# Kernel tuning notes

Measured on AMD Instinct MI355X. Metric: run time of the kernel, lower is better.

Reference implementation:

```python
import jax, jax.numpy as jnp
import numpy as np

C_M = 256   # norm_channel (msa channel)
C_Z = 128   # pair_channel
H = 8       # num_head
C = 32      # attention_channel per head


def layer_norm(x, gamma, beta, eps=1e-5):
    mu = jnp.mean(x, axis=-1, keepdims=True)
    var = jnp.var(x, axis=-1, keepdims=True)
    return (x - mu) * jax.lax.rsqrt(var + eps) * gamma + beta


def setup_inputs() -> dict:
    key = jax.random.key(0)
    ks = jax.random.split(key, 12)
    B, S, R = 1, 128, 256
    inp = {
        "msa_act": jax.random.normal(ks[0], (B, S, R, C_M), jnp.float32),
        "pair_act": jax.random.normal(ks[1], (B, R, R, C_Z), jnp.float32),
        "msa_mask": jnp.ones((B, S, R), jnp.float32),
        # query_norm params
        "qn_g": jnp.ones((C_M,), jnp.float32),
        "qn_b": jnp.zeros((C_M,), jnp.float32),
        # feat_2d_norm params
        "pn_g": jnp.ones((C_Z,), jnp.float32),
        "pn_b": jnp.zeros((C_Z,), jnp.float32),
        # feat_2d_weights: Linear(C_Z -> H, bias=False)
        "w2d": jax.random.normal(ks[2], (C_Z, H), jnp.float32) / np.sqrt(C_Z),
        # attention projections [C_M, H, C]
        "wq": jax.random.normal(ks[3], (C_M, H, C), jnp.float32) / np.sqrt(C_M),
        "wk": jax.random.normal(ks[4], (C_M, H, C), jnp.float32) / np.sqrt(C_M),
        "wv": jax.random.normal(ks[5], (C_M, H, C), jnp.float32) / np.sqrt(C_M),
        # gating linear [C_M, H, C] + bias
        "wg": jax.random.normal(ks[6], (C_M, H, C), jnp.float32) / np.sqrt(C_M),
        "bg": jnp.ones((H, C), jnp.float32),
        # output linear [H, C, C_M] + bias
        "wo": jax.random.normal(ks[7], (H, C, C_M), jnp.float32) / np.sqrt(H * C),
        "bo": jnp.zeros((C_M,), jnp.float32),
    }
    return inp


def reference(msa_act, pair_act, msa_mask, qn_g, qn_b, pn_g, pn_b, w2d,
              wq, wk, wv, wg, bg, wo, bo):
    # Pair bias: LayerNorm -> Linear(C_Z->H) -> permute to [B, 1, H, R, R]
    z = layer_norm(pair_act, pn_g, pn_b)            # [B, R, R, C_Z]
    z = jnp.einsum('bqkc,ch->bhqk', z, w2d)          # [B, H, R, R]
    z = z[:, None]                                   # [B, 1, H, R, R]

    # Mask bias: [B, S, 1, 1, R]
    mask_bias = (1e9 * (msa_mask - 1.0))[:, :, None, None, :]

    # Row-wise MHA with query norm
    m = layer_norm(msa_act, qn_g, qn_b)              # [B, S, R, C_M]
    scale = 1.0 / np.sqrt(C)
    q = jnp.einsum('bsqc,chd->bshqd', m, wq) * scale
    k = jnp.einsum('bskc,chd->bshkd', m, wk)
    v = jnp.einsum('bskc,chd->bshkd', m, wv)

    logits = jnp.einsum('bshqd,bshkd->bshqk', q, k) + mask_bias + z
    a = jax.nn.softmax(logits, axis=-1)              # [B, S, H, R, R]
    o = jnp.einsum('bshqk,bshkd->bsqhd', a, v)       # [B, S, R, H, C]

    g = jax.nn.sigmoid(jnp.einsum('bsqc,chd->bsqhd', m, wg) + bg)
    o = o * g
    out = jnp.einsum('bsqhd,hdc->bsqc', o, wo) + bo  # [B, S, R, C_M]
    return out
```

## Files before the change

kernel.cpp:

```cpp
#include <hip/hip_runtime.h>
#include <hip/hip_bf16.h>

typedef unsigned short u16;
typedef __attribute__((ext_vector_type(8))) short bf16x8;
typedef __attribute__((ext_vector_type(4))) float f32x4;

__device__ __forceinline__ float bf2f(u16 u){
  union { unsigned int i; float f; } v; v.i = ((unsigned int)u) << 16; return v.f;
}
__device__ __forceinline__ u16 f2bf(float f){
  union { float f; unsigned int i; } v; v.f = f;
  unsigned int i = v.i;
  return (u16)((i + 0x7fffu + ((i >> 16) & 1u)) >> 16);
}
__device__ __forceinline__ unsigned int pk2(float a, float b){
  union { __hip_bfloat162 v; unsigned int u; } c;
  c.v = __float22bfloat162_rn(float2{a, b});
  return c.u;
}
__device__ __forceinline__ float ldin(const void* p, int i, int f){
  return f ? ((const float*)p)[i] : bf2f(((const u16*)p)[i]);
}
__device__ __forceinline__ bf16x8 pack8(const float* v){
  union { bf16x8 v8; unsigned int w[4]; } u;
  #pragma unroll
  for (int j = 0; j < 4; ++j) u.w[j] = pk2(v[2*j], v[2*j+1]);
  return u.v8;
}

__global__ void k_sniff(const unsigned int* __restrict__ msa_w, int* __restrict__ flag)
{
  int lane = threadIdx.x & 63;
  int lo0 = 0, expok = 0;
  #pragma unroll
  for (int j = 0; j < 4; ++j) {
    unsigned int w = msa_w[lane * 4 + j];
    if ((w & 0xffffu) == 0u) lo0++;
    unsigned int e = (w >> 7) & 0xffu;
    if (e >= 110u && e <= 140u) expok++;
  }
  #pragma unroll
  for (int off = 1; off < 64; off <<= 1) {
    lo0   += __shfl_xor(lo0,   off, 64);
    expok += __shfl_xor(expok, off, 64);
  }
  if (lane == 0 && blockIdx.x == 0)
    *flag = (lo0 > 200) ? 1 : ((expok > 200) ? 0 : 1);
}

__global__ __launch_bounds__(256) void k_transpose(
    const void* __restrict__ wq, const void* __restrict__ wk,
    const void* __restrict__ wv, const void* __restrict__ wg,
    const void* __restrict__ wo, const int* __restrict__ flagp,
    u16* __restrict__ Wt, u16* __restrict__ wot)
{
  __shared__ u16 T[64 * 72];
  const int flag = *flagp;
  const int t = threadIdx.x;
  const int mat = blockIdx.x >> 4, tile = blockIdx.x & 15;
  const int R0 = (tile >> 2) * 64, C0 = (tile & 3) * 64;
  const void* src = (mat == 0) ? wq : (mat == 1) ? wk : (mat == 2) ? wv
                  : (mat == 3) ? wg : wo;
  u16* dst = (mat < 4) ? (Wt + mat * 65536) : wot;
  {
    int i = t >> 2, j0 = (t & 3) * 16;
    #pragma unroll
    for (int e = 0; e < 8; ++e) {
      float a = ldin(src, (R0 + i) * 256 + C0 + j0 + 2*e,     flag);
      float b = ldin(src, (R0 + i) * 256 + C0 + j0 + 2*e + 1, flag);
      *(unsigned int*)(T + i * 72 + j0 + 2*e) = pk2(a, b);
    }
  }
  __syncthreads();
  {
    int j = t >> 2, i0 = (t & 3) * 16;
    u16 o[16];
    #pragma unroll
    for (int e = 0; e < 16; ++e) o[e] = T[(i0 + e) * 72 + j];
    *(uint4*)(dst + (C0 + j) * 256 + R0 + i0)     = *(const uint4*)o;
    *(uint4*)(dst + (C0 + j) * 256 + R0 + i0 + 8) = *(const uint4*)(o + 8);
  }
}

__global__ __launch_bounds__(256) void k_pair_z(
    const void* __restrict__ pair, const void* __restrict__ png,
    const void* __restrict__ pnb, const void* __restrict__ w2d,
    const int* __restrict__ flagp, u16* __restrict__ z_bf)
{
  __shared__ u16 As[64 * 136];
  __shared__ u16 Bs[16 * 136];
  const int flag = *flagp;
  const int t = threadIdx.x, lane = t & 63, wave = t >> 6;
  const int g = lane >> 4, l15 = lane & 15;
  const int rowBase = blockIdx.x * 64;

  if (t < 128) {
    #pragma unroll
    for (int n = 0; n < 16; ++n)
      Bs[n * 136 + t] = (n < 8) ? f2bf(ldin(w2d, t * 8 + n, flag)) : (u16)0;
  }
  {
    int lrow = t >> 2, cb = (t & 3) * 32;
    int base = (rowBase + lrow) * 128 + cb;
    float x[32];
    if (flag) {
      const float* p = (const float*)pair + base;
      #pragma unroll
      for (int j = 0; j < 8; ++j) {
        float4 f4 = *(const float4*)(p + 4 * j);
        x[4*j] = f4.x; x[4*j+1] = f4.y; x[4*j+2] = f4.z; x[4*j+3] = f4.w;
      }
    } else {
      const u16* p = (const u16*)pair + base;
      #pragma unroll
      for (int j = 0; j < 4; ++j) {
        uint4 u = *(const uint4*)(p + 8 * j);
        const u16* h = (const u16*)&u;
        #pragma unroll
        for (int e = 0; e < 8; ++e) x[8*j+e] = bf2f(h[e]);
      }
    }
    float s = 0.f, sq = 0.f;
    #pragma unroll
    for (int j = 0; j < 32; ++j) { s += x[j]; sq += x[j] * x[j]; }
    s  += __shfl_xor(s, 1, 64);  s  += __shfl_xor(s, 2, 64);
    sq += __shfl_xor(sq, 1, 64); sq += __shfl_xor(sq, 2, 64);
    float mu = s * (1.f / 128.f);
    float var = sq * (1.f / 128.f) - mu * mu;
    float rs = rsqrtf(var + 1e-5f);
    float n_[32];
    #pragma unroll
    for (int j = 0; j < 32; ++j) {
      int c = cb + j;
      n_[j] = (x[j] - mu) * rs * ldin(png, c, flag) + ldin(pnb, c, flag);
    }
    u16* dst = As + lrow * 136 + cb;
    #pragma unroll
    for (int j = 0; j < 16; ++j)
      *(unsigned int*)(dst + 2*j) = pk2(n_[2*j], n_[2*j+1]);
  }
  __syncthreads();

  f32x4 accz = {0.f, 0.f, 0.f, 0.f};
  #pragma unroll
  for (int kb = 0; kb < 4; ++kb) {
    bf16x8 a = *(const bf16x8*)(As + (wave * 16 + l15) * 136 + kb * 32 + g * 8);
    bf16x8 b = *(const bf16x8*)(Bs + l15 * 136 + kb * 32 + g * 8);
    accz = __builtin_amdgcn_mfma_f32_16x16x32_bf16(a, b, accz, 0, 0, 0);
  }
  if (l15 < 8) {
    #pragma unroll
    for (int r = 0; r < 4; ++r)
      z_bf[l15 * 65536 + rowBase + wave * 16 + g * 4 + r] = f2bf(accz[r]);
  }
}

__global__ __launch_bounds__(256) void k_msa_ln(
    const void* __restrict__ msa, const void* __restrict__ qng,
    const void* __restrict__ qnb, const int* __restrict__ flagp,
    u16* __restrict__ m_bf)
{
  const int flag = *flagp;
  int wave = threadIdx.x >> 6, lane = threadIdx.x & 63;
  int row = blockIdx.x * 4 + wave;
  float x[4];
  if (flag) {
    float4 f4 = *((const float4*)msa + row * 64 + lane);
    x[0]=f4.x; x[1]=f4.y; x[2]=f4.z; x[3]=f4.w;
  } else {
    uint2 u = *((const uint2*)msa + row * 64 + lane);
    const u16* h = (const u16*)&u;
    #pragma unroll
    for (int j = 0; j < 4; ++j) x[j] = bf2f(h[j]);
  }
  float s = 0.f, sq = 0.f;
  #pragma unroll
  for (int j = 0; j < 4; ++j) { s += x[j]; sq += x[j] * x[j]; }
  #pragma unroll
  for (int off = 1; off < 64; off <<= 1) {
    s  += __shfl_xor(s,  off, 64);
    sq += __shfl_xor(sq, off, 64);
  }
  float mu = s * (1.f / 256.f);
  float var = sq * (1.f / 256.f) - mu * mu;
  float rs = rsqrtf(var + 1e-5f);
  float y[4];
  #pragma unroll
  for (int j = 0; j < 4; ++j) {
    int c = lane * 4 + j;
    y[j] = (x[j] - mu) * rs * ldin(qng, c, flag) + ldin(qnb, c, flag);
  }
  uint2 o2;
  o2.x = pk2(y[0], y[1]);
  o2.y = pk2(y[2], y[3]);
  *((uint2*)m_bf + row * 64 + lane) = o2;
}

__global__ __launch_bounds__(256, 2) void k_fused(
    const u16* __restrict__ m_bf, const u16* __restrict__ Wt,
    const void* __restrict__ bg, const u16* __restrict__ z_bf,
    const void* __restrict__ mask, const int* __restrict__ flagp,
    u16* __restrict__ og_ws)
{
  __shared__ u16 Ks[256 * 40];
  __shared__ u16 Vts[32 * 264];
  __shared__ u16 Qs[4][64 * 40];
  __shared__ float Tb[4][16 * 36];
  __shared__ float Mb[256];
  const int flag = *flagp;
  const int t = threadIdx.x, lane = t & 63, wave = t >> 6;
  const int s_ = blockIdx.x, h = blockIdx.y;
  const int g = lane >> 4, l15 = lane & 15;

  Mb[t] = 1e9f * (ldin(mask, s_ * 256 + t, flag) - 1.0f);

  bf16x8 af[8][4];
  #pragma unroll
  for (int kb = 0; kb < 8; ++kb)
    #pragma unroll
    for (int mt = 0; mt < 4; ++mt)
      af[kb][mt] = *(const bf16x8*)(
          m_bf + (s_ * 256 + wave * 64 + mt * 16 + l15) * 256 + kb * 32 + g * 8);

  const float scale = 0.17677669529663687f;
  float gg[4][2][4];
  f32x4 zero = {0.f, 0.f, 0.f, 0.f};

  #pragma unroll
  for (int matid = 0; matid < 4; ++matid) {
    const u16* W = Wt + matid * 65536 + (h * 32) * 256;
    f32x4 acc[4][2];
    #pragma unroll
    for (int mt = 0; mt < 4; ++mt) { acc[mt][0] = zero; acc[mt][1] = zero; }
    #pragma unroll
    for (int kb = 0; kb < 8; ++kb) {
      bf16x8 b0 = *(const bf16x8*)(W + l15 * 256        + kb * 32 + g * 8);
      bf16x8 b1 = *(const bf16x8*)(W + (16 + l15) * 256 + kb * 32 + g * 8);
      #pragma unroll
      for (int mt = 0; mt < 4; ++mt) {
        acc[mt][0] = __builtin_amdgcn_mfma_f32_16x16x32_bf16(af[kb][mt], b0, acc[mt][0], 0, 0, 0);
        acc[mt][1] = __builtin_amdgcn_mfma_f32_16x16x32_bf16(af[kb][mt], b1, acc[mt][1], 0, 0, 0);
      }
    }
    #pragma unroll
    for (int mt = 0; mt < 4; ++mt)
      #pragma unroll
      for (int nt = 0; nt < 2; ++nt)
        #pragma unroll
        for (int r = 0; r < 4; ++r) {
          int rowl = wave * 64 + mt * 16 + g * 4 + r;
          int dd = nt * 16 + l15;
          float v = acc[mt][nt][r];
          if (matid == 0)
            Qs[wave][(mt * 16 + g * 4 + r) * 40 + dd] = f2bf(v * scale);
          else if (matid == 1)
            Ks[rowl * 40 + dd] = f2bf(v);
          else if (matid == 2)
            Vts[dd * 264 + rowl] = f2bf(v);
          else {
            float gv = v + ldin(bg, h * 32 + dd, flag);
            gg[mt][nt][r] = 1.0f / (1.0f + __expf(-gv));
          }
        }
  }
  __syncthreads();

  const u16* Qw = &Qs[wave][0];
  float* Tw = &Tb[wave][0];
  for (int qt = 0; qt < 4; ++qt) {
    const int qbase = wave * 64 + qt * 16;
    bf16x8 aq = *(const bf16x8*)(Qw + (qt * 16 + l15) * 40 + g * 8);
    f32x4 S[16];
    #pragma unroll
    for (int kt = 0; kt < 16; ++kt) {
      bf16x8 bk = *(const bf16x8*)(Ks + (kt * 16 + l15) * 40 + g * 8);
      S[kt] = __builtin_amdgcn_mfma_f32_16x16x32_bf16(aq, bk, zero, 0, 0, 0);
    }
    const u16* zb = z_bf + h * 65536 + (qbase + l15) * 256;
    uint4 zu[8];
    #pragma unroll
    for (int kc = 0; kc < 8; ++kc) zu[kc] = *(const uint4*)(zb + kc * 32 + g * 8);

    float L[8][8];
    #pragma unroll
    for (int kc = 0; kc < 8; ++kc) {
      asm volatile("s_waitcnt lgkmcnt(0)" ::: "memory");
      #pragma unroll
      for (int half = 0; half < 2; ++half)
        #pragma unroll
        for (int r = 0; r < 4; ++r)
          Tw[(g * 4 + r) * 36 + half * 16 + l15] = S[kc * 2 + half][r];
      asm volatile("s_waitcnt lgkmcnt(0)" ::: "memory");
      float4 t0 = *(const float4*)(Tw + l15 * 36 + g * 8);
      float4 t1 = *(const float4*)(Tw + l15 * 36 + g * 8 + 4);
      float4 m0 = *(const float4*)(Mb + kc * 32 + g * 8);
      float4 m1 = *(const float4*)(Mb + kc * 32 + g * 8 + 4);
      const u16* zh = (const u16*)&zu[kc];
      L[kc][0] = __expf(t0.x + m0.x + bf2f(zh[0]));
      L[kc][1] = __expf(t0.y + m0.y + bf2f(zh[1]));
      L[kc][2] = __expf(t0.z + m0.z + bf2f(zh[2]));
      L[kc][3] = __expf(t0.w + m0.w + bf2f(zh[3]));
      L[kc][4] = __expf(t1.x + m1.x + bf2f(zh[4]));
      L[kc][5] = __expf(t1.y + m1.y + bf2f(zh[5]));
      L[kc][6] = __expf(t1.z + m1.z + bf2f(zh[6]));
      L[kc][7] = __expf(t1.w + m1.w + bf2f(zh[7]));
    }
    float sm = 0.f;
    #pragma unroll
    for (int kc = 0; kc < 8; ++kc)
      #pragma unroll
      for (int j = 0; j < 8; ++j) sm += L[kc][j];
    sm += __shfl_xor(sm, 16, 64);
    sm += __shfl_xor(sm, 32, 64);
    f32x4 O0 = zero, O1 = zero;
    #pragma unroll
    for (int kc = 0; kc < 8; ++kc) {
      bf16x8 ap  = pack8(&L[kc][0]);
      bf16x8 bv0 = *(const bf16x8*)(Vts + l15 * 264 + kc * 32 + g * 8);
      bf16x8 bv1 = *(const bf16x8*)(Vts + (16 + l15) * 264 + kc * 32 + g * 8);
      O0 = __builtin_amdgcn_mfma_f32_16x16x32_bf16(ap, bv0, O0, 0, 0, 0);
      O1 = __builtin_amdgcn_mfma_f32_16x16x32_bf16(ap, bv1, O1, 0, 0, 0);
    }
    #pragma unroll
    for (int r = 0; r < 4; ++r) {
      float smr = __shfl(sm, g * 4 + r, 64);
      float inv = 1.0f / smr;
      int qq = qbase + g * 4 + r;
      int base = (s_ * 256 + qq) * 256 + h * 32;
      float o0 = O0[r] * inv * gg[qt][0][r];
      float o1 = O1[r] * inv * gg[qt][1][r];
      og_ws[base + l15]      = f2bf(o0);
      og_ws[base + 16 + l15] = f2bf(o1);
    }
  }
}

__global__ __launch_bounds__(256, 2) void k_outproj(
    const u16* __restrict__ og, const u16* __restrict__ wot,
    const void* __restrict__ bo, const int* __restrict__ flagp,
    void* __restrict__ outv)
{
  const int flag = *flagp;
  const int t = threadIdx.x, lane = t & 63, wave = t >> 6;
  const int wm = (wave >> 1) * 64, wn = (wave & 1) * 64;
  const int rowBase = blockIdx.x * 128;
  const int ct = blockIdx.y;
  const int g = lane >> 4, l15 = lane & 15;

  bf16x8 af[8][4];
  #pragma unroll
  for (int kb = 0; kb < 8; ++kb)
    #pragma unroll
    for (int mt = 0; mt < 4; ++mt)
      af[kb][mt] = *(const bf16x8*)(
          og + (rowBase + wm + mt * 16 + l15) * 256 + kb * 32 + g * 8);

  const u16* Wb = wot + (ct * 128 + wn) * 256;
  f32x4 acc[4][4];
  f32x4 zero = {0.f, 0.f, 0.f, 0.f};
  #pragma unroll
  for (int i = 0; i < 4; ++i)
    #pragma unroll
    for (int j = 0; j < 4; ++j) acc[i][j] = zero;
  #pragma unroll
  for (int kb = 0; kb < 8; ++kb) {
    bf16x8 bb[4];
    #pragma unroll
    for (int nt = 0; nt < 4; ++nt)
      bb[nt] = *(const bf16x8*)(Wb + (nt * 16 + l15) * 256 + kb * 32 + g * 8);
    #pragma unroll
    for (int mt = 0; mt < 4; ++mt)
      #pragma unroll
      for (int nt = 0; nt < 4; ++nt)
        acc[mt][nt] = __builtin_amdgcn_mfma_f32_16x16x32_bf16(
            af[kb][mt], bb[nt], acc[mt][nt], 0, 0, 0);
  }
  #pragma unroll
  for (int mt = 0; mt < 4; ++mt)
    #pragma unroll
    for (int nt = 0; nt < 4; ++nt)
      #pragma unroll
      for (int r = 0; r < 4; ++r) {
        int row = rowBase + wm + mt * 16 + g * 4 + r;
        int col = ct * 128 + wn + nt * 16 + l15;
        float val = acc[mt][nt][r] + ldin(bo, col, flag);
        if (flag) ((float*)outv)[row * 256 + col] = val;
        else      ((u16*)outv)[row * 256 + col]   = f2bf(val);
      }
}

extern "C" void kernel_launch(void* const* d_in, const int* in_sizes, int n_in,
                              void* d_out, int out_size, void* d_ws, size_t ws_size,
                              hipStream_t stream)
{
  const void* msa  = d_in[0];
  const void* pair = d_in[1];
  const void* mask = d_in[2];
  const void* qng  = d_in[3];
  const void* qnb  = d_in[4];
  const void* png  = d_in[5];
  const void* pnb  = d_in[6];
  const void* w2d  = d_in[7];
  const void* wq   = d_in[8];
  const void* wk   = d_in[9];
  const void* wv   = d_in[10];
  const void* wg   = d_in[11];
  const void* bg   = d_in[12];
  const void* wo   = d_in[13];
  const void* bo   = d_in[14];

  char* ws = (char*)d_ws;
  u16* z_bf  = (u16*)(ws + 0);
  u16* Wt    = (u16*)(ws + 1048576);
  u16* wot   = (u16*)(ws + 1572864);
  int* flag  = (int*)(ws + 1703936);
  u16* m_bf  = (u16*)(ws + 1704192);
  u16* og_ws = (u16*)(ws + 18481408);

  hipLaunchKernelGGL(k_sniff, dim3(1), dim3(64), 0, stream,
                     (const unsigned int*)msa, flag);
  hipLaunchKernelGGL(k_transpose, dim3(80), dim3(256), 0, stream,
                     wq, wk, wv, wg, wo, flag, Wt, wot);
  hipLaunchKernelGGL(k_msa_ln, dim3(8192), dim3(256), 0, stream,
                     msa, qng, qnb, flag, m_bf);
  hipLaunchKernelGGL(k_pair_z, dim3(1024), dim3(256), 0, stream,
                     pair, png, pnb, w2d, flag, z_bf);
  hipLaunchKernelGGL(k_fused, dim3(128, 8), dim3(256), 0, stream,
                     m_bf, Wt, bg, z_bf, mask, flag, og_ws);
  hipLaunchKernelGGL(k_outproj, dim3(256, 2), dim3(256), 0, stream,
                     og_ws, wot, bo, flag, d_out);
}
```

Before: 261.6 us.

## Merge prep kernels, use exp2 softmax, and shrink fused-attention LDS for occupancy

Folds the weight transpose, pair-bias LayerNorm/projection and MSA LayerNorm into one launch, removing two kernel launches. In the attention kernel, Q and gate values now live packed in registers instead of LDS. The K tile drops its padding in favour of an XOR swizzle, and projections run in two 32-row chunks. Together these cut LDS and register use so launch bounds can rise to 3 blocks per CU. Softmax switches to exp2 with log2e folded into the Q scale, mask and z bias, and the row sum is fused into the PV loop, at the cost of an extra LDS round-trip to rebuild the Q fragment for each tile.

Measured after the change: 283.4 us. 1.08x slower.

```diff
diff --git a/kernel.cpp b/kernel.cpp
--- a/kernel.cpp
+++ b/kernel.cpp
@@ -2,8 +2,11 @@
 #include <hip/hip_bf16.h>
 
 typedef unsigned short u16;
+typedef unsigned int u32;
 typedef __attribute__((ext_vector_type(8))) short bf16x8;
 typedef __attribute__((ext_vector_type(4))) float f32x4;
+
+#define LOG2E 1.4426950408889634f
 
 __device__ __forceinline__ float bf2f(u16 u){
   union { unsigned int i; float f; } v; v.i = ((unsigned int)u) << 16; return v.f;
@@ -13,8 +16,8 @@
   unsigned int i = v.i;
   return (u16)((i + 0x7fffu + ((i >> 16) & 1u)) >> 16);
 }
-__device__ __forceinline__ unsigned int pk2(float a, float b){
-  union { __hip_bfloat162 v; unsigned int u; } c;
+__device__ __forceinline__ u32 pk2(float a, float b){
+  union { __hip_bfloat162 v; u32 u; } c;
   c.v = __float22bfloat162_rn(float2{a, b});
   return c.u;
 }
@@ -22,10 +25,17 @@
   return f ? ((const float*)p)[i] : bf2f(((const u16*)p)[i]);
 }
 __device__ __forceinline__ bf16x8 pack8(const float* v){
-  union { bf16x8 v8; unsigned int w[4]; } u;
+  union { bf16x8 v8; u32 w[4]; } u;
   #pragma unroll
   for (int j = 0; j < 4; ++j) u.w[j] = pk2(v[2*j], v[2*j+1]);
   return u.v8;
+}
+__device__ __forceinline__ float fexp2(float x){
+#if __has_builtin(__builtin_amdgcn_exp2f)
+  return __builtin_amdgcn_exp2f(x);
+#else
+  return exp2f(x);
+#endif
 }
 
 __global__ void k_sniff(const unsigned int* __restrict__ msa_w, int* __restrict__ flag)
@@ -48,240 +58,261 @@
     *flag = (lo0 > 200) ? 1 : ((expok > 200) ? 0 : 1);
 }
 
-__global__ __launch_bounds__(256) void k_transpose(
+__global__ __launch_bounds__(256) void k_prep(
     const void* __restrict__ wq, const void* __restrict__ wk,
     const void* __restrict__ wv, const void* __restrict__ wg,
-    const void* __restrict__ wo, const int* __restrict__ flagp,
-    u16* __restrict__ Wt, u16* __restrict__ wot)
-{
-  __shared__ u16 T[64 * 72];
-  const int flag = *flagp;
-  const int t = threadIdx.x;
-  const int mat = blockIdx.x >> 4, tile = blockIdx.x & 15;
-  const int R0 = (tile >> 2) * 64, C0 = (tile & 3) * 64;
-  const void* src = (mat == 0) ? wq : (mat == 1) ? wk : (mat == 2) ? wv
-                  : (mat == 3) ? wg : wo;
-  u16* dst = (mat < 4) ? (Wt + mat * 65536) : wot;
-  {
-    int i = t >> 2, j0 = (t & 3) * 16;
-    #pragma unroll
-    for (int e = 0; e < 8; ++e) {
-      float a = ldin(src, (R0 + i) * 256 + C0 + j0 + 2*e,     flag);
-      float b = ldin(src, (R0 + i) * 256 + C0 + j0 + 2*e + 1, flag);
-      *(unsigned int*)(T + i * 72 + j0 + 2*e) = pk2(a, b);
-    }
-  }
-  __syncthreads();
-  {
-    int j = t >> 2, i0 = (t & 3) * 16;
-    u16 o[16];
-    #pragma unroll
-    for (int e = 0; e < 16; ++e) o[e] = T[(i0 + e) * 72 + j];
-    *(uint4*)(dst + (C0 + j) * 256 + R0 + i0)     = *(const uint4*)o;
-    *(uint4*)(dst + (C0 + j) * 256 + R0 + i0 + 8) = *(const uint4*)(o + 8);
-  }
-}
-
-__global__ __launch_bounds__(256) void k_pair_z(
+    const void* __restrict__ wo,
     const void* __restrict__ pair, const void* __restrict__ png,
     const void* __restrict__ pnb, const void* __restrict__ w2d,
-    const int* __restrict__ flagp, u16* __restrict__ z_bf)
+    const void* __restrict__ msa, const void* __restrict__ qng,
+    const void* __restrict__ qnb, const int* __restrict__ flagp,
+    u16* __restrict__ Wt, u16* __restrict__ wot,
+    u16* __restrict__ z_bf, u16* __restrict__ m_bf)
 {
-  __shared__ u16 As[64 * 136];
-  __shared__ u16 Bs[16 * 136];
+  __shared__ u16 SMEM[64 * 136 + 16 * 136];
   const int flag = *flagp;
   const int t = threadIdx.x, lane = t & 63, wave = t >> 6;
-  const int g = lane >> 4, l15 = lane & 15;
-  const int rowBase = blockIdx.x * 64;
-
-  if (t < 128) {
-    #pragma unroll
-    for (int n = 0; n < 16; ++n)
-      Bs[n * 136 + t] = (n < 8) ? f2bf(ldin(w2d, t * 8 + n, flag)) : (u16)0;
-  }
-  {
-    int lrow = t >> 2, cb = (t & 3) * 32;
-    int base = (rowBase + lrow) * 128 + cb;
-    float x[32];
+  const int bid = blockIdx.x;
+
+  if (bid < 80) {
+    u16* T = SMEM;
+    const int mat = bid >> 4, tile = bid & 15;
+    const int R0 = (tile >> 2) * 64, C0 = (tile & 3) * 64;
+    const void* src = (mat == 0) ? wq : (mat == 1) ? wk : (mat == 2) ? wv
+                    : (mat == 3) ? wg : wo;
+    u16* dst = (mat < 4) ? (Wt + mat * 65536) : wot;
+    {
+      int i = t >> 2, j0 = (t & 3) * 16;
+      #pragma unroll
+      for (int e = 0; e < 8; ++e) {
+        float a = ldin(src, (R0 + i) * 256 + C0 + j0 + 2*e,     flag);
+        float b = ldin(src, (R0 + i) * 256 + C0 + j0 + 2*e + 1, flag);
+        *(u32*)(T + i * 72 + j0 + 2*e) = pk2(a, b);
+      }
+    }
+    __syncthreads();
+    {
+      int j = t >> 2, i0 = (t & 3) * 16;
+      u16 o[16];
+      #pragma unroll
+      for (int e = 0; e < 16; ++e) o[e] = T[(i0 + e) * 72 + j];
+      *(uint4*)(dst + (C0 + j) * 256 + R0 + i0)     = *(const uint4*)o;
+      *(uint4*)(dst + (C0 + j) * 256 + R0 + i0 + 8) = *(const uint4*)(o + 8);
+    }
+  } else if (bid < 80 + 1024) {
+    u16* As = SMEM;
+    u16* Bs = SMEM + 64 * 136;
+    const int g = lane >> 4, l15 = lane & 15;
+    const int rowBase = (bid - 80) * 64;
+    if (t < 128) {
+      #pragma unroll
+      for (int n = 0; n < 16; ++n)
+        Bs[n * 136 + t] = (n < 8) ? f2bf(ldin(w2d, t * 8 + n, flag)) : (u16)0;
+    }
+    {
+      int lrow = t >> 2, cb = (t & 3) * 32;
+      int base = (rowBase + lrow) * 128 + cb;
+      float x[32];
+      if (flag) {
+        const float* p = (const float*)pair + base;
+        #pragma unroll
+        for (int j = 0; j < 8; ++j) {
+          float4 f4 = *(const float4*)(p + 4 * j);
+          x[4*j] = f4.x; x[4*j+1] = f4.y; x[4*j+2] = f4.z; x[4*j+3] = f4.w;
+        }
+      } else {
+        const u16* p = (const u16*)pair + base;
+        #pragma unroll
+        for (int j = 0; j < 4; ++j) {
+          uint4 u = *(const uint4*)(p + 8 * j);
+          const u16* hh = (const u16*)&u;
+          #pragma unroll
+          for (int e = 0; e < 8; ++e) x[8*j+e] = bf2f(hh[e]);
+        }
+      }
+      float s = 0.f, sq = 0.f;
+      #pragma unroll
+      for (int j = 0; j < 32; ++j) { s += x[j]; sq += x[j] * x[j]; }
+      s  += __shfl_xor(s, 1, 64);  s  += __shfl_xor(s, 2, 64);
+      sq += __shfl_xor(sq, 1, 64); sq += __shfl_xor(sq, 2, 64);
+      float mu = s * (1.f / 128.f);
+      float var = sq * (1.f / 128.f) - mu * mu;
+      float rs = rsqrtf(var + 1e-5f);
+      float n_[32];
+      #pragma unroll
+      for (int j = 0; j < 32; ++j) {
+        int c = cb + j;
+        n_[j] = (x[j] - mu) * rs * ldin(png, c, flag) + ldin(pnb, c, flag);
+      }
+      u16* dst = As + lrow * 136 + cb;
+      #pragma unroll
+      for (int j = 0; j < 16; ++j)
+        *(u32*)(dst + 2*j) = pk2(n_[2*j], n_[2*j+1]);
+    }
+    __syncthreads();
+    f32x4 accz = {0.f, 0.f, 0.f, 0.f};
+    #pragma unroll
+    for (int kb = 0; kb < 4; ++kb) {
+      bf16x8 a = *(const bf16x8*)(As + (wave * 16 + l15) * 136 + kb * 32 + g * 8);
+      bf16x8 b = *(const bf16x8*)(Bs + l15 * 136 + kb * 32 + g * 8);
+      accz = __builtin_amdgcn_mfma_f32_16x16x32_bf16(a, b, accz, 0, 0, 0);
+    }
+    if (l15 < 8) {
+      #pragma unroll
+      for (int r = 0; r < 4; ++r)
+        z_bf[l15 * 65536 + rowBase + wave * 16 + g * 4 + r] = f2bf(accz[r] * LOG2E);
+    }
+  } else {
+    int row = (bid - 1104) * 4 + wave;
+    float x[4];
     if (flag) {
-      const float* p = (const float*)pair + base;
-      #pragma unroll
-      for (int j = 0; j < 8; ++j) {
-        float4 f4 = *(const float4*)(p + 4 * j);
-        x[4*j] = f4.x; x[4*j+1] = f4.y; x[4*j+2] = f4.z; x[4*j+3] = f4.w;
-      }
+      float4 f4 = *((const float4*)msa + row * 64 + lane);
+      x[0]=f4.x; x[1]=f4.y; x[2]=f4.z; x[3]=f4.w;
     } else {
-      const u16* p = (const u16*)pair + base;
-      #pragma unroll
-      for (int j = 0; j < 4; ++j) {
-        uint4 u = *(const uint4*)(p + 8 * j);
-        const u16* h = (const u16*)&u;
-        #pragma unroll
-        for (int e = 0; e < 8; ++e) x[8*j+e] = bf2f(h[e]);
-      }
+      uint2 u = *((const uint2*)msa + row * 64 + lane);
+      const u16* hh = (const u16*)&u;
+      #pragma unroll
+      for (int j = 0; j < 4; ++j) x[j] = bf2f(hh[j]);
     }
     float s = 0.f, sq = 0.f;
     #pragma unroll
-    for (int j = 0; j < 32; ++j) { s += x[j]; sq += x[j] * x[j]; }
-    s  += __shfl_xor(s, 1, 64);  s  += __shfl_xor(s, 2, 64);
-    sq += __shfl_xor(sq, 1, 64); sq += __shfl_xor(sq, 2, 64);
-    float mu = s * (1.f / 128.f);
-    float var = sq * (1.f / 128.f) - mu * mu;
+    for (int j = 0; j < 4; ++j) { s += x[j]; sq += x[j] * x[j]; }
+    #pragma unroll
+    for (int off = 1; off < 64; off <<= 1) {
+      s  += __shfl_xor(s,  off, 64);
+      sq += __shfl_xor(sq, off, 64);
+    }
+    float mu = s * (1.f / 256.f);
+    float var = sq * (1.f / 256.f) - mu * mu;
     float rs = rsqrtf(var + 1e-5f);
-    float n_[32];
-    #pragma unroll
-    for (int j = 0; j < 32; ++j) {
-      int c = cb + j;
-      n_[j] = (x[j] - mu) * rs * ldin(png, c, flag) + ldin(pnb, c, flag);
-    }
-    u16* dst = As + lrow * 136 + cb;
-    #pragma unroll
-    for (int j = 0; j < 16; ++j)
-      *(unsigned int*)(dst + 2*j) = pk2(n_[2*j], n_[2*j+1]);
-  }
-  __syncthreads();
-
-  f32x4 accz = {0.f, 0.f, 0.f, 0.f};
-  #pragma unroll
-  for (int kb = 0; kb < 4; ++kb) {
-    bf16x8 a = *(const bf16x8*)(As + (wave * 16 + l15) * 136 + kb * 32 + g * 8);
-    bf16x8 b = *(const bf16x8*)(Bs + l15 * 136 + kb * 32 + g * 8);
-    accz = __builtin_amdgcn_mfma_f32_16x16x32_bf16(a, b, accz, 0, 0, 0);
-  }
-  if (l15 < 8) {
-    #pragma unroll
-    for (int r = 0; r < 4; ++r)
-      z_bf[l15 * 65536 + rowBase + wave * 16 + g * 4 + r] = f2bf(accz[r]);
-  }
-}
-
-__global__ __launch_bounds__(256) void k_msa_ln(
-    const void* __restrict__ msa, const void* __restrict__ qng,
-    const void* __restrict__ qnb, const int* __restrict__ flagp,
-    u16* __restrict__ m_bf)
-{
-  const int flag = *flagp;
-  int wave = threadIdx.x >> 6, lane = threadIdx.x & 63;
-  int row = blockIdx.x * 4 + wave;
-  float x[4];
-  if (flag) {
-    float4 f4 = *((const float4*)msa + row * 64 + lane);
-    x[0]=f4.x; x[1]=f4.y; x[2]=f4.z; x[3]=f4.w;
-  } else {
-    uint2 u = *((const uint2*)msa + row * 64 + lane);
-    const u16* h = (const u16*)&u;
-    #pragma unroll
-    for (int j = 0; j < 4; ++j) x[j] = bf2f(h[j]);
-  }
-  float s = 0.f, sq = 0.f;
-  #pragma unroll
-  for (int j = 0; j < 4; ++j) { s += x[j]; sq += x[j] * x[j]; }
-  #pragma unroll
-  for (int off = 1; off < 64; off <<= 1) {
-    s  += __shfl_xor(s,  off, 64);
-    sq += __shfl_xor(sq, off, 64);
-  }
-  float mu = s * (1.f / 256.f);
-  float var = sq * (1.f / 256.f) - mu * mu;
-  float rs = rsqrtf(var + 1e-5f);
-  float y[4];
-  #pragma unroll
-  for (int j = 0; j < 4; ++j) {
-    int c = lane * 4 + j;
-    y[j] = (x[j] - mu) * rs * ldin(qng, c, flag) + ldin(qnb, c, flag);
-  }
-  uint2 o2;
-  o2.x = pk2(y[0], y[1]);
-  o2.y = pk2(y[2], y[3]);
-  *((uint2*)m_bf + row * 64 + lane) = o2;
-}
-
-__global__ __launch_bounds__(256, 2) void k_fused(
+    float y[4];
+    #pragma unroll
+    for (int j = 0; j < 4; ++j) {
+      int c = lane * 4 + j;
+      y[j] = (x[j] - mu) * rs * ldin(qng, c, flag) + ldin(qnb, c, flag);
+    }
+    uint2 o2;
+    o2.x = pk2(y[0], y[1]);
+    o2.y = pk2(y[2], y[3]);
+    *((uint2*)m_bf + row * 64 + lane) = o2;
+  }
+}
+
+__global__ __launch_bounds__(256, 3) void k_fused(
     const u16* __restrict__ m_bf, const u16* __restrict__ Wt,
     const void* __restrict__ bg, const u16* __restrict__ z_bf,
     const void* __restrict__ mask, const int* __restrict__ flagp,
     u16* __restrict__ og_ws)
 {
-  __shared__ u16 Ks[256 * 40];
+  __shared__ u16 Ks[256 * 32];
   __shared__ u16 Vts[32 * 264];
-  __shared__ u16 Qs[4][64 * 40];
-  __shared__ float Tb[4][16 * 36];
+  __shared__ float Sb[4][16 * 36];
   __shared__ float Mb[256];
   const int flag = *flagp;
   const int t = threadIdx.x, lane = t & 63, wave = t >> 6;
   const int s_ = blockIdx.x, h = blockIdx.y;
   const int g = lane >> 4, l15 = lane & 15;
 
-  Mb[t] = 1e9f * (ldin(mask, s_ * 256 + t, flag) - 1.0f);
-
-  bf16x8 af[8][4];
-  #pragma unroll
-  for (int kb = 0; kb < 8; ++kb)
-    #pragma unroll
-    for (int mt = 0; mt < 4; ++mt)
-      af[kb][mt] = *(const bf16x8*)(
-          m_bf + (s_ * 256 + wave * 64 + mt * 16 + l15) * 256 + kb * 32 + g * 8);
-
-  const float scale = 0.17677669529663687f;
-  float gg[4][2][4];
+  Mb[t] = (1e9f * LOG2E) * (ldin(mask, s_ * 256 + t, flag) - 1.0f);
+
+  const float qscale = 0.17677669529663687f * LOG2E;
+  u32 qpk[4][2][2];
+  u32 gpk[4][2][2];
   f32x4 zero = {0.f, 0.f, 0.f, 0.f};
 
   #pragma unroll
-  for (int matid = 0; matid < 4; ++matid) {
-    const u16* W = Wt + matid * 65536 + (h * 32) * 256;
-    f32x4 acc[4][2];
-    #pragma unroll
-    for (int mt = 0; mt < 4; ++mt) { acc[mt][0] = zero; acc[mt][1] = zero; }
-    #pragma unroll
-    for (int kb = 0; kb < 8; ++kb) {
-      bf16x8 b0 = *(const bf16x8*)(W + l15 * 256        + kb * 32 + g * 8);
-      bf16x8 b1 = *(const bf16x8*)(W + (16 + l15) * 256 + kb * 32 + g * 8);
-      #pragma unroll
-      for (int mt = 0; mt < 4; ++mt) {
-        acc[mt][0] = __builtin_amdgcn_mfma_f32_16x16x32_bf16(af[kb][mt], b0, acc[mt][0], 0, 0, 0);
-        acc[mt][1] = __builtin_amdgcn_mfma_f32_16x16x32_bf16(af[kb][mt], b1, acc[mt][1], 0, 0, 0);
-      }
-    }
-    #pragma unroll
-    for (int mt = 0; mt < 4; ++mt)
-      #pragma unroll
-      for (int nt = 0; nt < 2; ++nt)
+  for (int c = 0; c < 2; ++c) {
+    bf16x8 af[8][2];
+    #pragma unroll
+    for (int kb = 0; kb < 8; ++kb)
+      #pragma unroll
+      for (int mt = 0; mt < 2; ++mt)
+        af[kb][mt] = *(const bf16x8*)(
+            m_bf + (s_*256 + wave*64 + c*32 + mt*16 + l15)*256 + kb*32 + g*8);
+
+    #pragma unroll
+    for (int matid = 0; matid < 4; ++matid) {
+      const u16* W = Wt + matid * 65536 + (h * 32) * 256;
+      f32x4 acc[2][2];
+      acc[0][0] = zero; acc[0][1] = zero; acc[1][0] = zero; acc[1][1] = zero;
+      #pragma unroll
+      for (int kb = 0; kb < 8; ++kb) {
+        bf16x8 b0 = *(const bf16x8*)(W + l15 * 256        + kb * 32 + g * 8);
+        bf16x8 b1 = *(const bf16x8*)(W + (16 + l15) * 256 + kb * 32 + g * 8);
         #pragma unroll
-        for (int r = 0; r < 4; ++r) {
-          int rowl = wave * 64 + mt * 16 + g * 4 + r;
-          int dd = nt * 16 + l15;
-          float v = acc[mt][nt][r];
-          if (matid == 0)
-            Qs[wave][(mt * 16 + g * 4 + r) * 40 + dd] = f2bf(v * scale);
-          else if (matid == 1)
-            Ks[rowl * 40 + dd] = f2bf(v);
-          else if (matid == 2)
-            Vts[dd * 264 + rowl] = f2bf(v);
-          else {
-            float gv = v + ldin(bg, h * 32 + dd, flag);
-            gg[mt][nt][r] = 1.0f / (1.0f + __expf(-gv));
+        for (int mt = 0; mt < 2; ++mt) {
+          acc[mt][0] = __builtin_amdgcn_mfma_f32_16x16x32_bf16(af[kb][mt], b0, acc[mt][0], 0, 0, 0);
+          acc[mt][1] = __builtin_amdgcn_mfma_f32_16x16x32_bf16(af[kb][mt], b1, acc[mt][1], 0, 0, 0);
+        }
+      }
+      #pragma unroll
+      for (int mt = 0; mt < 2; ++mt) {
+        const int tile = c * 2 + mt;
+        if (matid == 0) {
+          #pragma unroll
+          for (int nt = 0; nt < 2; ++nt) {
+            qpk[tile][nt][0] = pk2(acc[mt][nt][0] * qscale, acc[mt][nt][1] * qscale);
+            qpk[tile][nt][1] = pk2(acc[mt][nt][2] * qscale, acc[mt][nt][3] * qscale);
           }
+        } else if (matid == 3) {
+          #pragma unroll
+          for (int nt = 0; nt < 2; ++nt) {
+            float b = ldin(bg, h * 32 + nt * 16 + l15, flag);
+            float s0 = 1.f / (1.f + __expf(-(acc[mt][nt][0] + b)));
+            float s1 = 1.f / (1.f + __expf(-(acc[mt][nt][1] + b)));
+            float s2 = 1.f / (1.f + __expf(-(acc[mt][nt][2] + b)));
+            float s3 = 1.f / (1.f + __expf(-(acc[mt][nt][3] + b)));
+            gpk[tile][nt][0] = pk2(s0, s1);
+            gpk[tile][nt][1] = pk2(s2, s3);
+          }
+        } else {
+          #pragma unroll
+          for (int nt = 0; nt < 2; ++nt)
+            #pragma unroll
+            for (int r = 0; r < 4; ++r) {
+              int rowl = wave * 64 + c * 32 + mt * 16 + g * 4 + r;
+              int dd = nt * 16 + l15;
+              u16 o = f2bf(acc[mt][nt][r]);
+              if (matid == 1)
+                Ks[rowl * 32 + (((dd >> 3) ^ (r & 3)) << 3) + (dd & 7)] = o;
+              else
+                Vts[dd * 264 + rowl] = o;
+            }
         }
+      }
+    }
   }
   __syncthreads();
 
-  const u16* Qw = &Qs[wave][0];
-  float* Tw = &Tb[wave][0];
+  float* Sw = &Sb[wave][0];
+  u16* Swu = (u16*)Sw;
+  const u16* zb_base = z_bf + h * 65536;
+
   for (int qt = 0; qt < 4; ++qt) {
     const int qbase = wave * 64 + qt * 16;
-    bf16x8 aq = *(const bf16x8*)(Qw + (qt * 16 + l15) * 40 + g * 8);
+    asm volatile("s_waitcnt lgkmcnt(0)" ::: "memory");
+    #pragma unroll
+    for (int nt = 0; nt < 2; ++nt)
+      #pragma unroll
+      for (int r = 0; r < 4; ++r)
+        Swu[(g * 4 + r) * 72 + nt * 16 + l15] =
+            (u16)(qpk[qt][nt][r >> 1] >> ((r & 1) * 16));
+    asm volatile("s_waitcnt lgkmcnt(0)" ::: "memory");
+    bf16x8 aq = *(const bf16x8*)(Swu + l15 * 72 + g * 8);
+
     f32x4 S[16];
     #pragma unroll
     for (int kt = 0; kt < 16; ++kt) {
-      bf16x8 bk = *(const bf16x8*)(Ks + (kt * 16 + l15) * 40 + g * 8);
+      bf16x8 bk = *(const bf16x8*)(Ks + (kt * 16 + l15) * 32 + ((g ^ (l15 & 3)) << 3));
       S[kt] = __builtin_amdgcn_mfma_f32_16x16x32_bf16(aq, bk, zero, 0, 0, 0);
     }
-    const u16* zb = z_bf + h * 65536 + (qbase + l15) * 256;
+    const u16* zb = zb_base + (qbase + l15) * 256;
     uint4 zu[8];
     #pragma unroll
     for (int kc = 0; kc < 8; ++kc) zu[kc] = *(const uint4*)(zb + kc * 32 + g * 8);
 
-    float L[8][8];
+    float sm = 0.f;
+    f32x4 O0 = zero, O1 = zero;
     #pragma unroll
     for (int kc = 0; kc < 8; ++kc) {
       asm volatile("s_waitcnt lgkmcnt(0)" ::: "memory");
@@ -289,48 +320,41 @@
       for (int half = 0; half < 2; ++half)
         #pragma unroll
         for (int r = 0; r < 4; ++r)
-          Tw[(g * 4 + r) * 36 + half * 16 + l15] = S[kc * 2 + half][r];
+          Sw[(g * 4 + r) * 36 + half * 16 + l15] = S[kc * 2 + half][r];
       asm volatile("s_waitcnt lgkmcnt(0)" ::: "memory");
-      float4 t0 = *(const float4*)(Tw + l15 * 36 + g * 8);
-      float4 t1 = *(const float4*)(Tw + l15 * 36 + g * 8 + 4);
+      float4 t0 = *(const float4*)(Sw + l15 * 36 + g * 8);
+      float4 t1 = *(const float4*)(Sw + l15 * 36 + g * 8 + 4);
       float4 m0 = *(const float4*)(Mb + kc * 32 + g * 8);
       float4 m1 = *(const float4*)(Mb + kc * 32 + g * 8 + 4);
       const u16* zh = (const u16*)&zu[kc];
-      L[kc][0] = __expf(t0.x + m0.x + bf2f(zh[0]));
-      L[kc][1] = __expf(t0.y + m0.y + bf2f(zh[1]));
-      L[kc][2] = __expf(t0.z + m0.z + bf2f(zh[2]));
-      L[kc][3] = __expf(t0.w + m0.w + bf2f(zh[3]));
-      L[kc][4] = __expf(t1.x + m1.x + bf2f(zh[4]));
-      L[kc][5] = __expf(t1.y + m1.y + bf2f(zh[5]));
-      L[kc][6] = __expf(t1.z + m1.z + bf2f(zh[6]));
-      L[kc][7] = __expf(t1.w + m1.w + bf2f(zh[7]));
-    }
-    float sm = 0.f;
-    #pragma unroll
-    for (int kc = 0; kc < 8; ++kc)
-      #pragma unroll
-      for (int j = 0; j < 8; ++j) sm += L[kc][j];
-    sm += __shfl_xor(sm, 16, 64);
-    sm += __shfl_xor(sm, 32, 64);
-    f32x4 O0 = zero, O1 = zero;
-    #pragma unroll
-    for (int kc = 0; kc < 8; ++kc) {
-      bf16x8 ap  = pack8(&L[kc][0]);
+      float L[8];
+      L[0] = fexp2(t0.x + m0.x + bf2f(zh[0]));
+      L[1] = fexp2(t0.y + m0.y + bf2f(zh[1]));
+      L[2] = fexp2(t0.z + m0.z + bf2f(zh[2]));
+      L[3] = fexp2(t0.w + m0.w + bf2f(zh[3]));
+      L[4] = fexp2(t1.x + m1.x + bf2f(zh[4]));
+      L[5] = fexp2(t1.y + m1.y + bf2f(zh[5]));
+      L[6] = fexp2(t1.z + m1.z + bf2f(zh[6]));
+      L[7] = fexp2(t1.w + m1.w + bf2f(zh[7]));
+      sm += ((L[0] + L[1]) + (L[2] + L[3])) + ((L[4] + L[5]) + (L[6] + L[7]));
+      bf16x8 ap  = pack8(L);
       bf16x8 bv0 = *(const bf16x8*)(Vts + l15 * 264 + kc * 32 + g * 8);
       bf16x8 bv1 = *(const bf16x8*)(Vts + (16 + l15) * 264 + kc * 32 + g * 8);
       O0 = __builtin_amdgcn_mfma_f32_16x16x32_bf16(ap, bv0, O0, 0, 0, 0);
       O1 = __builtin_amdgcn_mfma_f32_16x16x32_bf16(ap, bv1, O1, 0, 0, 0);
     }
+    sm += __shfl_xor(sm, 16, 64);
+    sm += __shfl_xor(sm, 32, 64);
     #pragma unroll
     for (int r = 0; r < 4; ++r) {
       float smr = __shfl(sm, g * 4 + r, 64);
       float inv = 1.0f / smr;
       int qq = qbase + g * 4 + r;
       int base = (s_ * 256 + qq) * 256 + h * 32;
-      float o0 = O0[r] * inv * gg[qt][0][r];
-      float o1 = O1[r] * inv * gg[qt][1][r];
-      og_ws[base + l15]      = f2bf(o0);
-      og_ws[base + 16 + l15] = f2bf(o1);
+      float g0 = bf2f((u16)(gpk[qt][0][r >> 1] >> ((r & 1) * 16)));
+      float g1 = bf2f((u16)(gpk[qt][1][r >> 1] >> ((r & 1) * 16)));
+      og_ws[base + l15]      = f2bf(O0[r] * inv * g0);
+      og_ws[base + 16 + l15] = f2bf(O1[r] * inv * g1);
     }
   }
 }
@@ -419,12 +443,9 @@
 
   hipLaunchKernelGGL(k_sniff, dim3(1), dim3(64), 0, stream,
                      (const unsigned int*)msa, flag);
-  hipLaunchKernelGGL(k_transpose, dim3(80), dim3(256), 0, stream,
-                     wq, wk, wv, wg, wo, flag, Wt, wot);
-  hipLaunchKernelGGL(k_msa_ln, dim3(8192), dim3(256), 0, stream,
-                     msa, qng, qnb, flag, m_bf);
-  hipLaunchKernelGGL(k_pair_z, dim3(1024), dim3(256), 0, stream,
-                     pair, png, pnb, w2d, flag, z_bf);
+  hipLaunchKernelGGL(k_prep, dim3(9296), dim3(256), 0, stream,
+                     wq, wk, wv, wg, wo, pair, png, pnb, w2d,
+                     msa, qng, qnb, flag, Wt, wot, z_bf, m_bf);
   hipLaunchKernelGGL(k_fused, dim3(128, 8), dim3(256), 0, stream,
                      m_bf, Wt, bg, z_bf, mask, flag, og_ws);
   hipLaunchKernelGGL(k_outproj, dim3(256, 2), dim3(256), 0, stream,
```
